# Kernel optimization log

Measured on AMD Instinct MI355X. Metric: run time of the kernel, lower is better.

## Reference

```python
import jax, jax.numpy as jnp
import numpy as np

DIM = 2048
N_HEADS = 16
N_KV_HEADS = 4
HEAD_DIM = DIM // N_HEADS  # 128
B, S = 2, 2048


def setup_inputs() -> dict:
    key = jax.random.key(0)
    ks = jax.random.split(key, 7)
    x = jax.random.normal(ks[0], (B, S, DIM), dtype=jnp.float32)
    # rotary tables: freqs_cis = exp(i * t * theta), theta_j = 1/10000^(2j/head_dim)
    inv_freq = 1.0 / (10000.0 ** (np.arange(0, HEAD_DIM, 2, dtype=np.float32) / HEAD_DIM))
    t = np.arange(S, dtype=np.float32)
    angles = jnp.asarray(np.outer(t, inv_freq))  # [S, HEAD_DIM//2]
    freqs_cos = jnp.cos(angles)
    freqs_sin = jnp.sin(angles)
    # Linear weights stored [in, out] (torch Linear applies x @ W.T; equivalent math)
    sd = 1.0 / np.sqrt(DIM)
    wq = jax.random.uniform(ks[1], (DIM, N_HEADS * HEAD_DIM), jnp.float32, -sd, sd)
    wk = jax.random.uniform(ks[2], (DIM, N_KV_HEADS * HEAD_DIM), jnp.float32, -sd, sd)
    wv = jax.random.uniform(ks[3], (DIM, N_KV_HEADS * HEAD_DIM), jnp.float32, -sd, sd)
    wo = jax.random.uniform(ks[4], (N_HEADS * HEAD_DIM, DIM), jnp.float32, -sd, sd)
    return {"x": x, "freqs_cos": freqs_cos, "freqs_sin": freqs_sin,
            "wq": wq, "wk": wk, "wv": wv, "wo": wo}


def _apply_rotary(xq, xk, cos, sin):
    # xq: [B,S,H,D], xk: [B,S,KH,D]; cos/sin: [S, D//2]
    def rot(t):
        tr = t.reshape(*t.shape[:-1], -1, 2)  # [..., D//2, 2] (real, imag)
        r, i = tr[..., 0], tr[..., 1]
        c = cos[None, :, None, :]
        s = sin[None, :, None, :]
        out_r = r * c - i * s
        out_i = r * s + i * c
        return jnp.stack([out_r, out_i], axis=-1).reshape(t.shape)
    return rot(xq), rot(xk)


def reference(x, freqs_cos, freqs_sin, wq, wk, wv, wo):
    bsz, seqlen, _ = x.shape
    xq = (x @ wq).reshape(bsz, seqlen, N_HEADS, HEAD_DIM)
    xk = (x @ wk).reshape(bsz, seqlen, N_KV_HEADS, HEAD_DIM)
    xv = (x @ wv).reshape(bsz, seqlen, N_KV_HEADS, HEAD_DIM)
    xq, xk = _apply_rotary(xq, xk, freqs_cos, freqs_sin)
    rep = N_HEADS // N_KV_HEADS
    xk = jnp.repeat(xk, rep, axis=2)
    xv = jnp.repeat(xv, rep, axis=2)
    # [B,H,S,D]
    q = xq.transpose(0, 2, 1, 3)
    k = xk.transpose(0, 2, 1, 3)
    v = xv.transpose(0, 2, 1, 3)
    scale = 1.0 / jnp.sqrt(jnp.asarray(HEAD_DIM, dtype=q.dtype))
    scores = jnp.einsum('bhqd,bhkd->bhqk', q, k) * scale
    causal = jnp.tril(jnp.ones((seqlen, seqlen), dtype=bool))
    scores = jnp.where(causal[None, None], scores, jnp.asarray(-jnp.inf, scores.dtype))
    attn = jax.nn.softmax(scores, axis=-1)
    out = jnp.einsum('bhqk,bhkd->bhqd', attn, v)  # [B,H,S,D]
    out = out.transpose(0, 2, 1, 3).reshape(bsz, seqlen, N_HEADS * HEAD_DIM)
    return out @ wo
```

## Files before the change

### kernel.cpp

```cpp
#include <hip/hip_runtime.h>
#include <hip/hip_bf16.h>

typedef unsigned short u16;
typedef unsigned int u32;
typedef __bf16 bf16x8 __attribute__((ext_vector_type(8)));
typedef float f32x4 __attribute__((ext_vector_type(4)));
typedef u32 u32x2 __attribute__((ext_vector_type(2)));

#define AS1 __attribute__((address_space(1)))
#define AS3 __attribute__((address_space(3)))

__device__ __forceinline__ void gload16(const void* gp, void* lp) {
    __builtin_amdgcn_global_load_lds((const AS1 u32*)gp, (AS3 u32*)lp, 16, 0, 0);
}

__device__ __forceinline__ u16 f2b(float f) {
    __bf16 h = (__bf16)f;
    return __builtin_bit_cast(u16, h);
}

__global__ __launch_bounds__(256) void cvt_kernel(const float* __restrict__ in,
                                                  u16* __restrict__ out, int n4) {
    int i = blockIdx.x * 256 + threadIdx.x;
    if (i < n4) {
        f32x4 v = *(const f32x4*)(in + (size_t)i * 4);
        u32x2 o;
        o[0] = (u32)f2b(v[0]) | ((u32)f2b(v[1]) << 16);
        o[1] = (u32)f2b(v[2]) | ((u32)f2b(v[3]) << 16);
        *(u32x2*)(out + (size_t)i * 4) = o;
    }
}

__global__ __launch_bounds__(256) void transpose_f32b(const float* __restrict__ in,
                                                      u16* __restrict__ out,
                                                      int R, int C) {
    __shared__ u16 tile[32][33];
    const int bx = blockIdx.x * 32;
    const int by = blockIdx.y * 32;
    const int tx = threadIdx.x & 31, ty = threadIdx.x >> 5;
#pragma unroll
    for (int i = 0; i < 32; i += 8)
        tile[ty + i][tx] = f2b(in[(size_t)(by + ty + i) * C + bx + tx]);
    __syncthreads();
#pragma unroll
    for (int i = 0; i < 32; i += 8)
        out[(size_t)(bx + ty + i) * R + by + tx] = tile[tx][ty + i];
}

__global__ __launch_bounds__(256) void transpose_v(const u16* __restrict__ qkv,
                                                   u16* __restrict__ vT) {
    __shared__ u16 tile[32][33];
    const int bx = blockIdx.x * 32;
    const int by = blockIdx.y * 32;
    const int tx = threadIdx.x & 31, ty = threadIdx.x >> 5;
#pragma unroll
    for (int i = 0; i < 32; i += 8)
        tile[ty + i][tx] = qkv[(size_t)(by + ty + i) * 3072 + 2560 + bx + tx];
    __syncthreads();
    const int b = by >> 11, s0 = by & 2047;
#pragma unroll
    for (int i = 0; i < 32; i += 8)
        vT[(size_t)(b * 512 + bx + ty + i) * 2048 + s0 + tx] = tile[tx][ty + i];
}

template <typename OT>
__global__ __launch_bounds__(256) void gemm_bt(const __bf16* __restrict__ A,
                                               const __bf16* __restrict__ Bt,
                                               OT* __restrict__ C,
                                               int K, int ldc) {
    __shared__ __align__(16) __bf16 Al[128 * 32];
    __shared__ __align__(16) __bf16 Bl[128 * 32];
    const int tid = threadIdx.x;
    const int lane = tid & 63, w = tid >> 6;
    const int wm = w >> 1, wn = w & 1;
    const int ln15 = lane & 15, lg = lane >> 4;
    const int bm = blockIdx.y, bn = blockIdx.x;

    const f32x4 fzero = {0.f, 0.f, 0.f, 0.f};
    f32x4 acc[4][4];
#pragma unroll
    for (int m = 0; m < 4; m++)
#pragma unroll
        for (int n = 0; n < 4; n++) acc[m][n] = fzero;

    const __bf16* Ab = A + (size_t)(bm * 128) * K;
    const __bf16* Bb = Bt + (size_t)(bn * 128) * K;

    for (int k0 = 0; k0 < K; k0 += 32) {
#pragma unroll
        for (int i = 0; i < 2; i++) {
            int gid = i * 256 + tid;
            int row = gid >> 2, gc = gid & 3;
            gload16(Ab + (size_t)row * K + k0 + gc * 8, (char*)Al + gid * 16);
            gload16(Bb + (size_t)row * K + k0 + gc * 8, (char*)Bl + gid * 16);
        }
        __syncthreads();
        bf16x8 af[4], bfr[4];
#pragma unroll
        for (int m = 0; m < 4; m++)
            af[m] = *(const bf16x8*)&Al[(wm * 64 + m * 16 + ln15) * 32 + lg * 8];
#pragma unroll
        for (int n = 0; n < 4; n++)
            bfr[n] = *(const bf16x8*)&Bl[(wn * 64 + n * 16 + ln15) * 32 + lg * 8];
#pragma unroll
        for (int m = 0; m < 4; m++)
#pragma unroll
            for (int n = 0; n < 4; n++)
                acc[m][n] = __builtin_amdgcn_mfma_f32_16x16x32_bf16(af[m], bfr[n], acc[m][n], 0, 0, 0);
        __syncthreads();
    }
#pragma unroll
    for (int m = 0; m < 4; m++)
#pragma unroll
        for (int n = 0; n < 4; n++)
#pragma unroll
            for (int r = 0; r < 4; r++) {
                int row = bm * 128 + wm * 64 + m * 16 + lg * 4 + r;
                int col = bn * 128 + wn * 64 + n * 16 + ln15;
                C[(size_t)row * ldc + col] = (OT)acc[m][n][r];
            }
}

__global__ __launch_bounds__(256) void rope_kernel(u32* __restrict__ qkv,
                                                   const float* __restrict__ fc,
                                                   const float* __restrict__ fs) {
    const int row = blockIdx.x;
    const int s = row & 2047;
    u32* base = qkv + (size_t)row * 1536;
    for (int i = threadIdx.x; i < 1280; i += 256) {
        const int h = i >> 6;
        const int p = i & 63;
        const int col2 = (h < 16) ? (h * 64 + p) : (1024 + (h - 16) * 64 + p);
        u32 v = base[col2];
        u32 lo = (v & 0xffffu) << 16, hi = v & 0xffff0000u;
        float xr = __builtin_bit_cast(float, lo);
        float xi = __builtin_bit_cast(float, hi);
        float c = fc[s * 64 + p];
        float si = fs[s * 64 + p];
        float o_r = xr * c - xi * si;
        float o_i = xr * si + xi * c;
        base[col2] = (u32)f2b(o_r) | ((u32)f2b(o_i) << 16);
    }
}

__global__ __launch_bounds__(256, 2) void attn_kernel(const __bf16* __restrict__ qkv,
                                                      const __bf16* __restrict__ vT,
                                                      __bf16* __restrict__ ctx) {
    __shared__ __align__(16) __bf16 Klds[2][64 * 128];
    __shared__ __align__(16) __bf16 VTlds[2][128 * 64];
    __shared__ __align__(16) __bf16 Plds[4][32 * 64];

    const int tid = threadIdx.x, lane = tid & 63, w = tid >> 6;
    const int ln15 = lane & 15, lg = lane >> 4;
    int i = blockIdx.x, qblk, hb;
    if (i < 256) { qblk = 15 - (i >> 5); hb = i & 31; }
    else { int j = i - 256; qblk = j >> 5; hb = j & 31; }
    const int h = hb >> 1, b = hb & 1;
    const int kvh = h >> 2;
    const int q0 = qblk * 128;
    const int qw0 = q0 + w * 32;
    const float c1 = 0.08838834764831845f * 1.4426950408889634f;

    const __bf16* qbase = qkv + (size_t)(b * 2048 + qw0 + ln15) * 3072 + h * 128;
    bf16x8 aq[2][4];
#pragma unroll
    for (int m = 0; m < 2; m++)
#pragma unroll
        for (int c = 0; c < 4; c++)
            aq[m][c] = *(const bf16x8*)(qbase + (size_t)m * 16 * 3072 + c * 32 + lg * 8);

    const __bf16* Kg = qkv + (size_t)(b * 2048) * 3072 + 2048 + kvh * 128;
    const __bf16* Vg = vT + (size_t)((b * 4 + kvh) * 128) * 2048;

    const f32x4 fzero = {0.f, 0.f, 0.f, 0.f};
    float m_run[2][4], l_run[2][4];
    f32x4 acc[2][8];
#pragma unroll
    for (int m = 0; m < 2; m++)
#pragma unroll
        for (int r = 0; r < 4; r++) { m_run[m][r] = -1e30f; l_run[m][r] = 0.f; }
#pragma unroll
    for (int m = 0; m < 2; m++)
#pragma unroll
        for (int dt = 0; dt < 8; dt++) acc[m][dt] = fzero;

    const int nt = 2 * qblk + 2;

#define STAGE(buf, t)                                                                     \
    do {                                                                                  \
        const int kb_ = (t) * 64;                                                         \
        _Pragma("unroll") for (int i2 = 0; i2 < 4; i2++) {                                \
            int gid = i2 * 256 + tid;                                                     \
            int kv = gid >> 4, sl = gid & 15;                                             \
            gload16(Kg + (size_t)(kb_ + kv) * 3072 + ((sl ^ (kv & 7)) * 8),               \
                    (char*)Klds[buf] + gid * 16);                                         \
        }                                                                                 \
        _Pragma("unroll") for (int i2 = 0; i2 < 4; i2++) {                                \
            int gid = i2 * 256 + tid;                                                     \
            int d = gid >> 3, sl = gid & 7;                                               \
            gload16(Vg + (size_t)d * 2048 + kb_ + ((sl ^ (d & 7)) * 8),                   \
                    (char*)VTlds[buf] + gid * 16);                                        \
        }                                                                                 \
    } while (0)

    STAGE(0, 0);
    __syncthreads();

    for (int t = 0; t < nt; t++) {
        const int cur = t & 1;
        const int kbase = t * 64;
        if (t + 1 < nt) STAGE(cur ^ 1, t + 1);

        if (kbase <= qw0 + 31) {
            f32x4 st[2][4];
#pragma unroll
            for (int ct = 0; ct < 4; ct++) {
                int kv = ct * 16 + ln15;
                f32x4 s0 = fzero, s1 = fzero;
#pragma unroll
                for (int c = 0; c < 4; c++) {
                    int g = c * 4 + lg;
                    bf16x8 bk = *(const bf16x8*)&Klds[cur][kv * 128 + ((g ^ (kv & 7)) * 8)];
                    s0 = __builtin_amdgcn_mfma_f32_16x16x32_bf16(aq[0][c], bk, s0, 0, 0, 0);
                    s1 = __builtin_amdgcn_mfma_f32_16x16x32_bf16(aq[1][c], bk, s1, 0, 0, 0);
                }
                st[0][ct] = s0;
                st[1][ct] = s1;
            }
            if (kbase + 63 > qw0) {
#pragma unroll
                for (int m = 0; m < 2; m++)
#pragma unroll
                    for (int ct = 0; ct < 4; ct++) {
                        int kvi = kbase + ct * 16 + ln15;
#pragma unroll
                        for (int r = 0; r < 4; r++) {
                            int qi = qw0 + m * 16 + lg * 4 + r;
                            if (kvi > qi) st[m][ct][r] = -1e30f;
                        }
                    }
            }
#pragma unroll
            for (int m = 0; m < 2; m++)
#pragma unroll
                for (int r = 0; r < 4; r++) {
                    float m0 = fmaxf(fmaxf(st[m][0][r], st[m][1][r]), fmaxf(st[m][2][r], st[m][3][r]));
#pragma unroll
                    for (int off = 1; off < 16; off <<= 1) m0 = fmaxf(m0, __shfl_xor(m0, off, 16));
                    float mn = fmaxf(m_run[m][r], m0);
                    float corr = exp2f((m_run[m][r] - mn) * c1);
                    m_run[m][r] = mn;
                    const int q = m * 16 + lg * 4 + r;
                    float sm = 0.f;
#pragma unroll
                    for (int ct = 0; ct < 4; ct++) {
                        float p = exp2f((st[m][ct][r] - mn) * c1);
                        sm += p;
                        int pg = ct * 2 + (ln15 >> 3);
                        Plds[w][q * 64 + ((pg ^ (q & 7)) * 8) + (ln15 & 7)] = (__bf16)p;
                    }
#pragma unroll
                    for (int off = 1; off < 16; off <<= 1) sm += __shfl_xor(sm, off, 16);
                    l_run[m][r] = l_run[m][r] * corr + sm;
#pragma unroll
                    for (int dt = 0; dt < 8; dt++) acc[m][dt][r] *= corr;
                }
#pragma unroll
            for (int s2 = 0; s2 < 2; s2++) {
                const int kvg = s2 * 4 + lg;
                bf16x8 pa0 = *(const bf16x8*)&Plds[w][(0 * 16 + ln15) * 64 + ((kvg ^ (ln15 & 7)) * 8)];
                bf16x8 pa1 = *(const bf16x8*)&Plds[w][(1 * 16 + ln15) * 64 + ((kvg ^ (ln15 & 7)) * 8)];
#pragma unroll
                for (int dt = 0; dt < 8; dt++) {
                    int d = dt * 16 + ln15;
                    bf16x8 bv = *(const bf16x8*)&VTlds[cur][d * 64 + ((kvg ^ (d & 7)) * 8)];
                    acc[0][dt] = __builtin_amdgcn_mfma_f32_16x16x32_bf16(pa0, bv, acc[0][dt], 0, 0, 0);
                    acc[1][dt] = __builtin_amdgcn_mfma_f32_16x16x32_bf16(pa1, bv, acc[1][dt], 0, 0, 0);
                }
            }
        }
        __syncthreads();
    }
#undef STAGE

    __bf16* crow = ctx + (size_t)(b * 2048 + qw0) * 2048 + h * 128;
#pragma unroll
    for (int m = 0; m < 2; m++)
#pragma unroll
        for (int dt = 0; dt < 8; dt++)
#pragma unroll
            for (int r = 0; r < 4; r++) {
                float v = acc[m][dt][r] / l_run[m][r];
                crow[(size_t)(m * 16 + lg * 4 + r) * 2048 + dt * 16 + ln15] = (__bf16)v;
            }
}

extern "C" void kernel_launch(void* const* d_in, const int* in_sizes, int n_in,
                              void* d_out, int out_size, void* d_ws, size_t ws_size,
                              hipStream_t stream) {
    const float* x = (const float*)d_in[0];
    const float* fc = (const float*)d_in[1];
    const float* fs = (const float*)d_in[2];
    const float* wq = (const float*)d_in[3];
    const float* wk = (const float*)d_in[4];
    const float* wv = (const float*)d_in[5];
    const float* wo = (const float*)d_in[6];
    float* out = (float*)d_out;

    char* ws = (char*)d_ws;
    __bf16* wT  = (__bf16*)ws;
    __bf16* woT = (__bf16*)(ws + 12582912);
    __bf16* xb  = (__bf16*)(ws + 20971520);
    __bf16* qkv = (__bf16*)(ws + 37748736);
    __bf16* ctx = (__bf16*)(ws + 62914560);
    __bf16* vT  = xb;

    cvt_kernel<<<8192, 256, 0, stream>>>(x, (u16*)xb, 2097152);

    transpose_f32b<<<dim3(64, 64), 256, 0, stream>>>(wq, (u16*)wT, 2048, 2048);
    transpose_f32b<<<dim3(16, 64), 256, 0, stream>>>(wk, (u16*)(wT + 2048 * 2048), 2048, 512);
    transpose_f32b<<<dim3(16, 64), 256, 0, stream>>>(wv, (u16*)(wT + 2560 * 2048), 2048, 512);
    transpose_f32b<<<dim3(64, 64), 256, 0, stream>>>(wo, (u16*)woT, 2048, 2048);

    gemm_bt<__bf16><<<dim3(24, 32), 256, 0, stream>>>(xb, wT, qkv, 2048, 3072);

    rope_kernel<<<4096, 256, 0, stream>>>((u32*)qkv, fc, fs);

    transpose_v<<<dim3(16, 128), 256, 0, stream>>>((const u16*)qkv, (u16*)vT);

    attn_kernel<<<512, 256, 0, stream>>>(qkv, vT, ctx);

    gemm_bt<float><<<dim3(16, 32), 256, 0, stream>>>(ctx, woT, out, 2048, 2048);
}
```

Measured before the change: 382.9 us.

## Merge prep kernels, fuse RoPE into QKV GEMM, swizzle tiles, shrink P buffer

Folds the x conversion and the four weight transposes into a single prep launch, and applies rotary embedding in the QKV GEMM epilogue using lane shuffles, so the separate RoPE pass over qkv goes away. The GEMM now remaps workgroup ids with a swizzle to improve L2 reuse. In attention, the P tile is staged per 16-row half in a smaller LDS buffer, which cuts LDS use but serialises the two m halves through the same buffer. RoPE is now applied to fp32 accumulators before the bf16 rounding, which slightly changes numerics.

```diff
diff --git a/kernel.cpp b/kernel.cpp
--- a/kernel.cpp
+++ b/kernel.cpp
@@ -19,32 +19,42 @@
     return __builtin_bit_cast(u16, h);
 }
 
-__global__ __launch_bounds__(256) void cvt_kernel(const float* __restrict__ in,
-                                                  u16* __restrict__ out, int n4) {
-    int i = blockIdx.x * 256 + threadIdx.x;
-    if (i < n4) {
-        f32x4 v = *(const f32x4*)(in + (size_t)i * 4);
+__global__ __launch_bounds__(256) void prep_kernel(const float* __restrict__ x,
+                                                   const float* __restrict__ wq,
+                                                   const float* __restrict__ wk,
+                                                   const float* __restrict__ wv,
+                                                   const float* __restrict__ wo,
+                                                   u16* __restrict__ xb,
+                                                   u16* __restrict__ wT,
+                                                   u16* __restrict__ woT) {
+    __shared__ u16 tile[32][33];
+    const int bid = blockIdx.x, tid = threadIdx.x;
+    if (bid < 8192) {
+        int i = bid * 256 + tid;
+        f32x4 v = *(const f32x4*)(x + (size_t)i * 4);
         u32x2 o;
         o[0] = (u32)f2b(v[0]) | ((u32)f2b(v[1]) << 16);
         o[1] = (u32)f2b(v[2]) | ((u32)f2b(v[3]) << 16);
-        *(u32x2*)(out + (size_t)i * 4) = o;
+        *(u32x2*)(xb + (size_t)i * 4) = o;
+        return;
     }
-}
-
-__global__ __launch_bounds__(256) void transpose_f32b(const float* __restrict__ in,
-                                                      u16* __restrict__ out,
-                                                      int R, int C) {
-    __shared__ u16 tile[32][33];
-    const int bx = blockIdx.x * 32;
-    const int by = blockIdx.y * 32;
-    const int tx = threadIdx.x & 31, ty = threadIdx.x >> 5;
+    const float* in;
+    u16* out;
+    int C, t;
+    if (bid < 12288) { t = bid - 8192; in = wq; out = wT; C = 2048; }
+    else if (bid < 13312) { t = bid - 12288; in = wk; out = wT + 2048 * 2048; C = 512; }
+    else if (bid < 14336) { t = bid - 13312; in = wv; out = wT + 2560 * 2048; C = 512; }
+    else { t = bid - 14336; in = wo; out = woT; C = 2048; }
+    const int nbx = C >> 5;
+    const int bx = (t % nbx) * 32, by = (t / nbx) * 32;
+    const int tx = tid & 31, ty = tid >> 5;
 #pragma unroll
     for (int i = 0; i < 32; i += 8)
         tile[ty + i][tx] = f2b(in[(size_t)(by + ty + i) * C + bx + tx]);
     __syncthreads();
 #pragma unroll
     for (int i = 0; i < 32; i += 8)
-        out[(size_t)(bx + ty + i) * R + by + tx] = tile[tx][ty + i];
+        out[(size_t)(bx + ty + i) * 2048 + by + tx] = tile[tx][ty + i];
 }
 
 __global__ __launch_bounds__(256) void transpose_v(const u16* __restrict__ qkv,
@@ -63,18 +73,23 @@
         vT[(size_t)(b * 512 + bx + ty + i) * 2048 + s0 + tx] = tile[tx][ty + i];
 }
 
-template <typename OT>
+template <typename OT, bool ROPE>
 __global__ __launch_bounds__(256) void gemm_bt(const __bf16* __restrict__ A,
                                                const __bf16* __restrict__ Bt,
                                                OT* __restrict__ C,
-                                               int K, int ldc) {
+                                               int K, int ldc,
+                                               const float* __restrict__ fc,
+                                               const float* __restrict__ fs) {
     __shared__ __align__(16) __bf16 Al[128 * 32];
     __shared__ __align__(16) __bf16 Bl[128 * 32];
     const int tid = threadIdx.x;
     const int lane = tid & 63, w = tid >> 6;
     const int wm = w >> 1, wn = w & 1;
     const int ln15 = lane & 15, lg = lane >> 4;
-    const int bm = blockIdx.y, bn = blockIdx.x;
+    const int nwg = gridDim.x * gridDim.y;
+    const int lid = blockIdx.y * gridDim.x + blockIdx.x;
+    const int swz = (lid & 7) * (nwg >> 3) + (lid >> 3);
+    const int bm = swz / gridDim.x, bn = swz % gridDim.x;
 
     const f32x4 fzero = {0.f, 0.f, 0.f, 0.f};
     f32x4 acc[4][4];
@@ -109,6 +124,30 @@
                 acc[m][n] = __builtin_amdgcn_mfma_f32_16x16x32_bf16(af[m], bfr[n], acc[m][n], 0, 0, 0);
         __syncthreads();
     }
+
+    if (ROPE) {
+#pragma unroll
+        for (int n = 0; n < 4; n++) {
+            const int col = bn * 128 + wn * 64 + n * 16 + ln15;
+            if (col < 2560) {
+                const int p = (col & 127) >> 1;
+                const bool odd = (col & 1) != 0;
+#pragma unroll
+                for (int m = 0; m < 4; m++)
+#pragma unroll
+                    for (int r = 0; r < 4; r++) {
+                        const int row = bm * 128 + wm * 64 + m * 16 + lg * 4 + r;
+                        const int sp = row & 2047;
+                        float c = fc[sp * 64 + p];
+                        float sn = fs[sp * 64 + p];
+                        float v = acc[m][n][r];
+                        float v2 = __shfl_xor(v, 1);
+                        acc[m][n][r] = odd ? (v2 * sn + v * c) : (v * c - v2 * sn);
+                    }
+            }
+        }
+    }
+
 #pragma unroll
     for (int m = 0; m < 4; m++)
 #pragma unroll
@@ -119,28 +158,6 @@
                 int col = bn * 128 + wn * 64 + n * 16 + ln15;
                 C[(size_t)row * ldc + col] = (OT)acc[m][n][r];
             }
-}
-
-__global__ __launch_bounds__(256) void rope_kernel(u32* __restrict__ qkv,
-                                                   const float* __restrict__ fc,
-                                                   const float* __restrict__ fs) {
-    const int row = blockIdx.x;
-    const int s = row & 2047;
-    u32* base = qkv + (size_t)row * 1536;
-    for (int i = threadIdx.x; i < 1280; i += 256) {
-        const int h = i >> 6;
-        const int p = i & 63;
-        const int col2 = (h < 16) ? (h * 64 + p) : (1024 + (h - 16) * 64 + p);
-        u32 v = base[col2];
-        u32 lo = (v & 0xffffu) << 16, hi = v & 0xffff0000u;
-        float xr = __builtin_bit_cast(float, lo);
-        float xi = __builtin_bit_cast(float, hi);
-        float c = fc[s * 64 + p];
-        float si = fs[s * 64 + p];
-        float o_r = xr * c - xi * si;
-        float o_i = xr * si + xi * c;
-        base[col2] = (u32)f2b(o_r) | ((u32)f2b(o_i) << 16);
-    }
 }
 
 __global__ __launch_bounds__(256, 2) void attn_kernel(const __bf16* __restrict__ qkv,
@@ -148,7 +165,7 @@
                                                       __bf16* __restrict__ ctx) {
     __shared__ __align__(16) __bf16 Klds[2][64 * 128];
     __shared__ __align__(16) __bf16 VTlds[2][128 * 64];
-    __shared__ __align__(16) __bf16 Plds[4][32 * 64];
+    __shared__ __align__(16) __bf16 Plds[4][16 * 64];
 
     const int tid = threadIdx.x, lane = tid & 63, w = tid >> 6;
     const int ln15 = lane & 15, lg = lane >> 4;
@@ -241,7 +258,7 @@
                     }
             }
 #pragma unroll
-            for (int m = 0; m < 2; m++)
+            for (int m = 0; m < 2; m++) {
 #pragma unroll
                 for (int r = 0; r < 4; r++) {
                     float m0 = fmaxf(fmaxf(st[m][0][r], st[m][1][r]), fmaxf(st[m][2][r], st[m][3][r]));
@@ -250,7 +267,7 @@
                     float mn = fmaxf(m_run[m][r], m0);
                     float corr = exp2f((m_run[m][r] - mn) * c1);
                     m_run[m][r] = mn;
-                    const int q = m * 16 + lg * 4 + r;
+                    const int q = lg * 4 + r;
                     float sm = 0.f;
 #pragma unroll
                     for (int ct = 0; ct < 4; ct++) {
@@ -266,16 +283,15 @@
                     for (int dt = 0; dt < 8; dt++) acc[m][dt][r] *= corr;
                 }
 #pragma unroll
-            for (int s2 = 0; s2 < 2; s2++) {
-                const int kvg = s2 * 4 + lg;
-                bf16x8 pa0 = *(const bf16x8*)&Plds[w][(0 * 16 + ln15) * 64 + ((kvg ^ (ln15 & 7)) * 8)];
-                bf16x8 pa1 = *(const bf16x8*)&Plds[w][(1 * 16 + ln15) * 64 + ((kvg ^ (ln15 & 7)) * 8)];
-#pragma unroll
-                for (int dt = 0; dt < 8; dt++) {
-                    int d = dt * 16 + ln15;
-                    bf16x8 bv = *(const bf16x8*)&VTlds[cur][d * 64 + ((kvg ^ (d & 7)) * 8)];
-                    acc[0][dt] = __builtin_amdgcn_mfma_f32_16x16x32_bf16(pa0, bv, acc[0][dt], 0, 0, 0);
-                    acc[1][dt] = __builtin_amdgcn_mfma_f32_16x16x32_bf16(pa1, bv, acc[1][dt], 0, 0, 0);
+                for (int s2 = 0; s2 < 2; s2++) {
+                    const int kvg = s2 * 4 + lg;
+                    bf16x8 pa = *(const bf16x8*)&Plds[w][ln15 * 64 + ((kvg ^ (ln15 & 7)) * 8)];
+#pragma unroll
+                    for (int dt = 0; dt < 8; dt++) {
+                        int d = dt * 16 + ln15;
+                        bf16x8 bv = *(const bf16x8*)&VTlds[cur][d * 64 + ((kvg ^ (d & 7)) * 8)];
+                        acc[m][dt] = __builtin_amdgcn_mfma_f32_16x16x32_bf16(pa, bv, acc[m][dt], 0, 0, 0);
+                    }
                 }
             }
         }
@@ -315,20 +331,13 @@
     __bf16* ctx = (__bf16*)(ws + 62914560);
     __bf16* vT  = xb;
 
-    cvt_kernel<<<8192, 256, 0, stream>>>(x, (u16*)xb, 2097152);
-
-    transpose_f32b<<<dim3(64, 64), 256, 0, stream>>>(wq, (u16*)wT, 2048, 2048);
-    transpose_f32b<<<dim3(16, 64), 256, 0, stream>>>(wk, (u16*)(wT + 2048 * 2048), 2048, 512);
-    transpose_f32b<<<dim3(16, 64), 256, 0, stream>>>(wv, (u16*)(wT + 2560 * 2048), 2048, 512);
-    transpose_f32b<<<dim3(64, 64), 256, 0, stream>>>(wo, (u16*)woT, 2048, 2048);
-
-    gemm_bt<__bf16><<<dim3(24, 32), 256, 0, stream>>>(xb, wT, qkv, 2048, 3072);
-
-    rope_kernel<<<4096, 256, 0, stream>>>((u32*)qkv, fc, fs);
+    prep_kernel<<<18432, 256, 0, stream>>>(x, wq, wk, wv, wo, (u16*)xb, (u16*)wT, (u16*)woT);
+
+    gemm_bt<__bf16, true><<<dim3(24, 32), 256, 0, stream>>>(xb, wT, qkv, 2048, 3072, fc, fs);
 
     transpose_v<<<dim3(16, 128), 256, 0, stream>>>((const u16*)qkv, (u16*)vT);
 
     attn_kernel<<<512, 256, 0, stream>>>(qkv, vT, ctx);
 
-    gemm_bt<float><<<dim3(16, 32), 256, 0, stream>>>(ctx, woT, out, 2048, 2048);
-}
+    gemm_bt<float, false><<<dim3(16, 32), 256, 0, stream>>>(ctx, woT, out, 2048, 2048, nullptr, nullptr);
+}
```

Result: slower. 410.3 us (+7.2%).
